# Kernel tuning notes

Measured on AMD Instinct MI355X. Metric: run time of the kernel, lower is better.

The kernel has to match this reference:

```python
import jax, jax.numpy as jnp
import numpy as np

B, S, D, FF, E = 4, 2048, 1024, 4096, 8


def setup_inputs() -> dict:
    key = jax.random.key(0)
    ks = jax.random.split(key, 6)
    scale_r = 1.0 / np.sqrt(D)
    return {
        "x": jax.random.normal(ks[0], (B, S, D), dtype=jnp.float32),
        "W_router": jax.random.normal(ks[1], (D, E), dtype=jnp.float32) * scale_r,
        "W1": jax.random.normal(ks[2], (E, D, FF), dtype=jnp.float32) * (1.0 / np.sqrt(D)),
        "b1": jnp.zeros((E, FF), dtype=jnp.float32),
        "W2": jax.random.normal(ks[3], (E, FF, D), dtype=jnp.float32) * (1.0 / np.sqrt(FF)),
        "b2": jnp.zeros((E, D), dtype=jnp.float32),
    }


def reference(x, W_router, W1, b1, W2, b2):
    # Router: softmax over experts, top-2, renormalize the 2 gates with softmax
    logits = jnp.einsum("bsd,de->bse", x, W_router)          # [B,S,E]
    probs = jax.nn.softmax(logits, axis=-1)
    top_vals, top_idx = jax.lax.top_k(probs, 2)               # [B,S,2]
    gates2 = jax.nn.softmax(top_vals, axis=-1)                # [B,S,2]

    num_experts = W1.shape[0]
    out = jnp.zeros_like(x)
    # Faithful masked-dense MoE: each expert runs over all tokens (input masked),
    # output scaled by its gate (0 for non-selected tokens).
    for i in range(num_experts):
        sel = (top_idx == i)                                  # [B,S,2] bool
        mask = jnp.any(sel, axis=-1, keepdims=True).astype(x.dtype)  # [B,S,1]
        xi = x * mask
        h = jax.nn.gelu(jnp.einsum("bsd,df->bsf", xi, W1[i]) + b1[i], approximate=False)
        yi = jnp.einsum("bsf,fd->bsd", h, W2[i]) + b2[i]
        g = jnp.sum(gates2 * sel.astype(x.dtype), axis=-1, keepdims=True)  # [B,S,1]
        out = out + yi * g
    return out
```

## Files before the change

kernel.cpp:

```cpp
#include <hip/hip_runtime.h>
#include <hip/hip_bf16.h>
#include <math.h>

#define NEXP 8
#define DDIM 1024
#define FFDIM 4096
#define NTOK 8192
#define NSLOT (NTOK * 2)
#define BM 128
#define BN 128
#define BK 64
#define MAXT ((NSLOT / BM) + NEXP)

typedef __attribute__((ext_vector_type(8))) __bf16 bf16x8;
typedef __attribute__((ext_vector_type(4))) float f32x4;

union BF8 { __bf16 b[8]; uint4 u; bf16x8 v; };

__device__ __forceinline__ float gelu_exact(float v) {
    return 0.5f * v * (1.0f + erff(v * 0.70710678118654752f));
}

__device__ __forceinline__ int swz(int row, int colb) {
    return row * 128 + (colb ^ ((row & 7) << 4));
}

__global__ __launch_bounds__(64)
void router_kernel(const float* __restrict__ x, const float* __restrict__ Wr,
                   int* __restrict__ idx2, float* __restrict__ gates2,
                   int* __restrict__ counts)
{
    int t = blockIdx.x;
    int lane = threadIdx.x;
    const float* xr = x + (size_t)t * DDIM;
    float acc[NEXP];
#pragma unroll
    for (int e = 0; e < NEXP; ++e) acc[e] = 0.f;
    for (int d = lane; d < DDIM; d += 64) {
        float xv = xr[d];
        const float* wrow = Wr + d * NEXP;
#pragma unroll
        for (int e = 0; e < NEXP; ++e) acc[e] += xv * wrow[e];
    }
#pragma unroll
    for (int e = 0; e < NEXP; ++e) {
        float v = acc[e];
        for (int off = 32; off > 0; off >>= 1) v += __shfl_xor(v, off, 64);
        acc[e] = v;
    }
    if (lane == 0) {
        float mx = acc[0];
#pragma unroll
        for (int e = 1; e < NEXP; ++e) mx = fmaxf(mx, acc[e]);
        float p[NEXP]; float s = 0.f;
#pragma unroll
        for (int e = 0; e < NEXP; ++e) { p[e] = expf(acc[e] - mx); s += p[e]; }
        float inv = 1.f / s;
#pragma unroll
        for (int e = 0; e < NEXP; ++e) p[e] *= inv;
        int i1 = 0; float p1 = p[0];
#pragma unroll
        for (int e = 1; e < NEXP; ++e) if (p[e] > p1) { p1 = p[e]; i1 = e; }
        int i2 = -1; float p2 = -1.f;
#pragma unroll
        for (int e = 0; e < NEXP; ++e) {
            if (e == i1) continue;
            if (p[e] > p2) { p2 = p[e]; i2 = e; }
        }
        float u = expf(p2 - p1);
        float den = 1.f + u;
        idx2[2 * t] = i1; idx2[2 * t + 1] = i2;
        gates2[2 * t] = 1.f / den; gates2[2 * t + 1] = u / den;
        atomicAdd(&counts[i1], 1);
        atomicAdd(&counts[i2], 1);
    }
}

__global__ void offsets_kernel(const int* __restrict__ counts, int* __restrict__ offsets,
                               int* __restrict__ cursors, int* __restrict__ tiletab)
{
    if (threadIdx.x != 0 || blockIdx.x != 0) return;
    int off = 0, idx = 0;
    for (int e = 0; e < NEXP; ++e) {
        offsets[e] = off;
        cursors[e] = 0;
        int nt = (counts[e] + BM - 1) / BM;
        for (int t = 0; t < nt; ++t) { tiletab[2 * idx] = e; tiletab[2 * idx + 1] = t; ++idx; }
        off += counts[e];
    }
    for (; idx < MAXT; ++idx) { tiletab[2 * idx] = -1; tiletab[2 * idx + 1] = 0; }
}

__global__ __launch_bounds__(256)
void fill_kernel(const int* __restrict__ idx2, const float* __restrict__ gates2,
                 const int* __restrict__ offsets, int* __restrict__ cursors,
                 int* __restrict__ perm, float* __restrict__ gate_slot)
{
    int t = blockIdx.x * 256 + threadIdx.x;
    if (t >= NTOK) return;
#pragma unroll
    for (int s = 0; s < 2; ++s) {
        int e = idx2[2 * t + s];
        int pos = atomicAdd(&cursors[e], 1);
        int slot = offsets[e] + pos;
        perm[slot] = t;
        gate_slot[slot] = gates2[2 * t + s];
    }
}

__global__ __launch_bounds__(256)
void convert_x_kernel(const float* __restrict__ x, __bf16* __restrict__ xb)
{
    size_t i = ((size_t)blockIdx.x * 256 + threadIdx.x) * 8;
    float4 a = *(const float4*)(x + i);
    float4 b = *(const float4*)(x + i + 4);
    BF8 pk;
    pk.b[0] = (__bf16)a.x; pk.b[1] = (__bf16)a.y; pk.b[2] = (__bf16)a.z; pk.b[3] = (__bf16)a.w;
    pk.b[4] = (__bf16)b.x; pk.b[5] = (__bf16)b.y; pk.b[6] = (__bf16)b.z; pk.b[7] = (__bf16)b.w;
    *(uint4*)(xb + i) = pk.u;
}

__global__ __launch_bounds__(256)
void convert_w_kernel(const float* __restrict__ W, __bf16* __restrict__ WT, int K, int N)
{
    int ktiles = K >> 6;
    int nt = blockIdx.x / ktiles;
    int kt = blockIdx.x % ktiles;
    int e = blockIdx.y;
    const float* We = W + (size_t)e * K * N;
    int t = threadIdx.x;
    int r = t & 127;
    int khalf = t >> 7;
    const float* src = We + (size_t)(kt * 64 + khalf * 32) * N + nt * 128 + r;
    char* dst = (char*)WT + ((((size_t)e * (N >> 7) + nt) * ktiles + kt) << 14);
    float f[32];
#pragma unroll
    for (int j = 0; j < 32; ++j) f[j] = src[(size_t)j * N];
#pragma unroll
    for (int i = 0; i < 4; ++i) {
        BF8 pk;
#pragma unroll
        for (int q = 0; q < 8; ++q) pk.b[q] = (__bf16)f[i * 8 + q];
        int gi = khalf * 4 + i;
        *(uint4*)(dst + r * 128 + ((gi * 16) ^ ((r & 7) << 4))) = pk.u;
    }
}

__device__ __forceinline__ bool tile_header(const int* counts, const int* offsets,
                                            const int* tiletab, int e_arg, int c_arg, int CH,
                                            int& e, int& start, int& cnt, int& hbase, int& row0,
                                            int& rows_here)
{
    int rowtile;
    if (e_arg >= 0) {
        e = e_arg;
        int cbase = c_arg * CH;
        cnt = counts[e] - cbase;
        if (cnt <= 0) return false;
        if (cnt > CH) cnt = CH;
        start = offsets[e] + cbase;
        rowtile = blockIdx.y;
        hbase = start;
    } else {
        e = tiletab[2 * blockIdx.y];
        if (e < 0) return false;
        rowtile = tiletab[2 * blockIdx.y + 1];
        start = offsets[e];
        cnt = counts[e];
        hbase = 0;
    }
    row0 = rowtile * BM;
    if (row0 >= cnt) return false;
    rows_here = cnt - row0;
    if (rows_here > BM) rows_here = BM;
    return true;
}

__global__ __launch_bounds__(256)
void gemm1_fast(const __bf16* __restrict__ xb, const __bf16* __restrict__ W1T,
                const float* __restrict__ b1,
                const int* __restrict__ perm, const int* __restrict__ counts,
                const int* __restrict__ offsets, const int* __restrict__ tiletab,
                __bf16* __restrict__ H, int e_arg, int c_arg, int CH)
{
    __shared__ __align__(16) char smem[(BM + BN) * 128];
    char* As = smem;
    char* Bs = smem + BM * 128;

    int e, start, cnt, hbase, row0, rows_here;
    if (!tile_header(counts, offsets, tiletab, e_arg, c_arg, CH, e, start, cnt, hbase, row0, rows_here))
        return;

    const float* b1e = b1 + (size_t)e * FFDIM;
    int nt = blockIdx.x;
    int n0 = nt * BN;
    const char* bsrc = (const char*)W1T + ((((size_t)e * (FFDIM >> 7) + nt) * (DDIM >> 6)) << 14);

    int tid = threadIdx.x;
    int lane = tid & 63;
    int wid = tid >> 6;
    int wm = wid >> 1, wn = wid & 1;
    int lr = lane & 15, lhi = lane >> 4;

    int ar = tid >> 1, ach = tid & 1;
    int token = -1;
    if (ar < rows_here) token = perm[start + row0 + ar];
    const __bf16* arow = xb + (size_t)(token < 0 ? 0 : token) * DDIM + ach * 32;

    int boff = wid * 4096 + lane * 16;

    f32x4 acc[4][4] = {};

    for (int kt = 0; kt < DDIM / BK; ++kt) {
        __syncthreads();
        {
            uint4 v[4];
            if (token >= 0) {
                const uint4* p = (const uint4*)(arow + kt * BK);
#pragma unroll
                for (int i = 0; i < 4; ++i) v[i] = p[i];
            } else {
#pragma unroll
                for (int i = 0; i < 4; ++i) v[i] = make_uint4(0u, 0u, 0u, 0u);
            }
#pragma unroll
            for (int i = 0; i < 4; ++i)
                *(uint4*)(As + swz(ar, ach * 64 + i * 16)) = v[i];
        }
        {
            const char* tsrc = bsrc + ((size_t)kt << 14);
#pragma unroll
            for (int j = 0; j < 4; ++j) {
                uint4 v = *(const uint4*)(tsrc + j * 1024 + boff);
                *(uint4*)(Bs + j * 1024 + boff) = v;
            }
        }
        __syncthreads();

#pragma unroll
        for (int kk = 0; kk < 2; ++kk) {
            bf16x8 af[4], bfr[4];
#pragma unroll
            for (int m = 0; m < 4; ++m)
                af[m] = *(const bf16x8*)(As + swz(wm * 64 + m * 16 + lr, kk * 64 + lhi * 16));
#pragma unroll
            for (int n = 0; n < 4; ++n)
                bfr[n] = *(const bf16x8*)(Bs + swz(wn * 64 + n * 16 + lr, kk * 64 + lhi * 16));
#pragma unroll
            for (int m = 0; m < 4; ++m)
#pragma unroll
                for (int n = 0; n < 4; ++n)
                    acc[m][n] = __builtin_amdgcn_mfma_f32_16x16x32_bf16(af[m], bfr[n], acc[m][n], 0, 0, 0);
        }
    }

    float bias[4];
#pragma unroll
    for (int n = 0; n < 4; ++n) bias[n] = b1e[n0 + wn * 64 + n * 16 + lr];

#pragma unroll
    for (int m = 0; m < 4; ++m) {
        int rbase = wm * 64 + m * 16 + lhi * 4;
#pragma unroll
        for (int j = 0; j < 4; ++j) {
            int rl = rbase + j;
            if (rl < rows_here) {
                __bf16* hr = H + (size_t)(start + row0 + rl - hbase) * FFDIM + n0 + wn * 64;
#pragma unroll
                for (int n = 0; n < 4; ++n) {
                    float v = acc[m][n][j] + bias[n];
                    hr[n * 16 + lr] = (__bf16)gelu_exact(v);
                }
            }
        }
    }
}

__global__ __launch_bounds__(256)
void gemm2_fast(const __bf16* __restrict__ H, const __bf16* __restrict__ W2T,
                const float* __restrict__ b2,
                const int* __restrict__ perm, const float* __restrict__ gate_slot,
                const int* __restrict__ counts, const int* __restrict__ offsets,
                const int* __restrict__ tiletab,
                float* __restrict__ out, int e_arg, int c_arg, int CH)
{
    __shared__ __align__(16) char smem[(BM + BN) * 128];
    char* As = smem;
    char* Bs = smem + BM * 128;

    int e, start, cnt, hbase, row0, rows_here;
    if (!tile_header(counts, offsets, tiletab, e_arg, c_arg, CH, e, start, cnt, hbase, row0, rows_here))
        return;

    const float* b2e = b2 + (size_t)e * DDIM;
    int nt = blockIdx.x;
    int n0 = nt * BN;
    const char* bsrc = (const char*)W2T + ((((size_t)e * (DDIM >> 7) + nt) * (FFDIM >> 6)) << 14);

    int tid = threadIdx.x;
    int lane = tid & 63;
    int wid = tid >> 6;
    int wm = wid >> 1, wn = wid & 1;
    int lr = lane & 15, lhi = lane >> 4;

    int ar = tid >> 1, ach = tid & 1;
    bool aval = (ar < rows_here);
    const __bf16* hrow = H + (size_t)(aval ? (start + row0 + ar - hbase) : 0) * FFDIM + ach * 32;

    int boff = wid * 4096 + lane * 16;

    f32x4 acc[4][4] = {};

    for (int kt = 0; kt < FFDIM / BK; ++kt) {
        __syncthreads();
        {
            uint4 v[4];
            if (aval) {
                const uint4* p = (const uint4*)(hrow + kt * BK);
#pragma unroll
                for (int i = 0; i < 4; ++i) v[i] = p[i];
            } else {
#pragma unroll
                for (int i = 0; i < 4; ++i) v[i] = make_uint4(0u, 0u, 0u, 0u);
            }
#pragma unroll
            for (int i = 0; i < 4; ++i)
                *(uint4*)(As + swz(ar, ach * 64 + i * 16)) = v[i];
        }
        {
            const char* tsrc = bsrc + ((size_t)kt << 14);
#pragma unroll
            for (int j = 0; j < 4; ++j) {
                uint4 v = *(const uint4*)(tsrc + j * 1024 + boff);
                *(uint4*)(Bs + j * 1024 + boff) = v;
            }
        }
        __syncthreads();

#pragma unroll
        for (int kk = 0; kk < 2; ++kk) {
            bf16x8 af[4], bfr[4];
#pragma unroll
            for (int m = 0; m < 4; ++m)
                af[m] = *(const bf16x8*)(As + swz(wm * 64 + m * 16 + lr, kk * 64 + lhi * 16));
#pragma unroll
            for (int n = 0; n < 4; ++n)
                bfr[n] = *(const bf16x8*)(Bs + swz(wn * 64 + n * 16 + lr, kk * 64 + lhi * 16));
#pragma unroll
            for (int m = 0; m < 4; ++m)
#pragma unroll
                for (int n = 0; n < 4; ++n)
                    acc[m][n] = __builtin_amdgcn_mfma_f32_16x16x32_bf16(af[m], bfr[n], acc[m][n], 0, 0, 0);
        }
    }

    float bias[4];
#pragma unroll
    for (int n = 0; n < 4; ++n) bias[n] = b2e[n0 + wn * 64 + n * 16 + lr];

#pragma unroll
    for (int m = 0; m < 4; ++m) {
        int rbase = wm * 64 + m * 16 + lhi * 4;
#pragma unroll
        for (int j = 0; j < 4; ++j) {
            int rl = rbase + j;
            if (rl < rows_here) {
                int slot = start + row0 + rl;
                int token = perm[slot];
                float g = gate_slot[slot];
                float* orow = out + (size_t)token * DDIM + n0 + wn * 64;
#pragma unroll
                for (int n = 0; n < 4; ++n) {
                    float v = (acc[m][n][j] + bias[n]) * g;
                    atomicAdd(orow + n * 16 + lr, v);
                }
            }
        }
    }
}

__global__ __launch_bounds__(256)
void gemm1_legacy(const float* __restrict__ x, const float* __restrict__ W1,
                  const float* __restrict__ b1,
                  const int* __restrict__ perm, const int* __restrict__ counts,
                  const int* __restrict__ offsets, const int* __restrict__ tiletab,
                  __bf16* __restrict__ H, int e_arg, int c_arg, int CH)
{
    __shared__ __align__(16) char smem[(BM + BN) * 128];
    char* As = smem;
    char* Bs = smem + BM * 128;

    int e, start, cnt, hbase, row0, rows_here;
    if (!tile_header(counts, offsets, tiletab, e_arg, c_arg, CH, e, start, cnt, hbase, row0, rows_here))
        return;

    const float* W1e = W1 + (size_t)e * DDIM * FFDIM;
    const float* b1e = b1 + (size_t)e * FFDIM;
    int n0 = blockIdx.x * BN;

    int tid = threadIdx.x;
    int lane = tid & 63;
    int wid = tid >> 6;
    int wm = wid >> 1, wn = wid & 1;
    int lr = lane & 15, lhi = lane >> 4;

    int ar = tid >> 1, ach = tid & 1;
    int token = -1;
    if (ar < rows_here) token = perm[start + row0 + ar];
    const float* arow = x + (size_t)(token < 0 ? 0 : token) * DDIM + ach * 32;

    int bn = tid & 127, bkh = tid >> 7;
    const float* bcol = W1e + (size_t)bkh * 32 * FFDIM + n0 + bn;

    f32x4 acc[4][4] = {};

    for (int k0 = 0; k0 < DDIM; k0 += BK) {
        __syncthreads();
        {
            BF8 pk[4];
            if (token >= 0) {
                const float4* p = (const float4*)(arow + k0);
#pragma unroll
                for (int i = 0; i < 4; ++i) {
                    float4 v0 = p[2 * i], v1 = p[2 * i + 1];
                    pk[i].b[0] = (__bf16)v0.x; pk[i].b[1] = (__bf16)v0.y;
                    pk[i].b[2] = (__bf16)v0.z; pk[i].b[3] = (__bf16)v0.w;
                    pk[i].b[4] = (__bf16)v1.x; pk[i].b[5] = (__bf16)v1.y;
                    pk[i].b[6] = (__bf16)v1.z; pk[i].b[7] = (__bf16)v1.w;
                }
            } else {
#pragma unroll
                for (int i = 0; i < 4; ++i) pk[i].u = make_uint4(0u, 0u, 0u, 0u);
            }
#pragma unroll
            for (int i = 0; i < 4; ++i)
                *(uint4*)(As + swz(ar, ach * 64 + i * 16)) = pk[i].u;
        }
        {
            float f[32];
            const float* p = bcol + (size_t)k0 * FFDIM;
#pragma unroll
            for (int j = 0; j < 32; ++j) f[j] = p[(size_t)j * FFDIM];
#pragma unroll
            for (int i = 0; i < 4; ++i) {
                BF8 pk;
#pragma unroll
                for (int q = 0; q < 8; ++q) pk.b[q] = (__bf16)f[i * 8 + q];
                *(uint4*)(Bs + swz(bn, bkh * 64 + i * 16)) = pk.u;
            }
        }
        __syncthreads();

#pragma unroll
        for (int kk = 0; kk < 2; ++kk) {
            bf16x8 af[4], bfr[4];
#pragma unroll
            for (int m = 0; m < 4; ++m)
                af[m] = *(const bf16x8*)(As + swz(wm * 64 + m * 16 + lr, kk * 64 + lhi * 16));
#pragma unroll
            for (int n = 0; n < 4; ++n)
                bfr[n] = *(const bf16x8*)(Bs + swz(wn * 64 + n * 16 + lr, kk * 64 + lhi * 16));
#pragma unroll
            for (int m = 0; m < 4; ++m)
#pragma unroll
                for (int n = 0; n < 4; ++n)
                    acc[m][n] = __builtin_amdgcn_mfma_f32_16x16x32_bf16(af[m], bfr[n], acc[m][n], 0, 0, 0);
        }
    }

    float bias[4];
#pragma unroll
    for (int n = 0; n < 4; ++n) bias[n] = b1e[n0 + wn * 64 + n * 16 + lr];

#pragma unroll
    for (int m = 0; m < 4; ++m) {
        int rbase = wm * 64 + m * 16 + lhi * 4;
#pragma unroll
        for (int j = 0; j < 4; ++j) {
            int rl = rbase + j;
            if (rl < rows_here) {
                __bf16* hr = H + (size_t)(start + row0 + rl - hbase) * FFDIM + n0 + wn * 64;
#pragma unroll
                for (int n = 0; n < 4; ++n) {
                    float v = acc[m][n][j] + bias[n];
                    hr[n * 16 + lr] = (__bf16)gelu_exact(v);
                }
            }
        }
    }
}

__global__ __launch_bounds__(256)
void gemm2_legacy(const __bf16* __restrict__ H, const float* __restrict__ W2,
                  const float* __restrict__ b2,
                  const int* __restrict__ perm, const float* __restrict__ gate_slot,
                  const int* __restrict__ counts, const int* __restrict__ offsets,
                  const int* __restrict__ tiletab,
                  float* __restrict__ out, int e_arg, int c_arg, int CH)
{
    __shared__ __align__(16) char smem[(BM + BN) * 128];
    char* As = smem;
    char* Bs = smem + BM * 128;

    int e, start, cnt, hbase, row0, rows_here;
    if (!tile_header(counts, offsets, tiletab, e_arg, c_arg, CH, e, start, cnt, hbase, row0, rows_here))
        return;

    const float* W2e = W2 + (size_t)e * FFDIM * DDIM;
    const float* b2e = b2 + (size_t)e * DDIM;
    int n0 = blockIdx.x * BN;

    int tid = threadIdx.x;
    int lane = tid & 63;
    int wid = tid >> 6;
    int wm = wid >> 1, wn = wid & 1;
    int lr = lane & 15, lhi = lane >> 4;

    int ar = tid >> 1, ach = tid & 1;
    bool aval = (ar < rows_here);
    const __bf16* hrow = H + (size_t)(aval ? (start + row0 + ar - hbase) : 0) * FFDIM + ach * 32;

    int bn = tid & 127, bkh = tid >> 7;
    const float* bcol = W2e + (size_t)bkh * 32 * DDIM + n0 + bn;

    f32x4 acc[4][4] = {};

    for (int k0 = 0; k0 < FFDIM; k0 += BK) {
        __syncthreads();
        {
            uint4 v[4];
            if (aval) {
                const uint4* p = (const uint4*)(hrow + k0);
#pragma unroll
                for (int i = 0; i < 4; ++i) v[i] = p[i];
            } else {
#pragma unroll
                for (int i = 0; i < 4; ++i) v[i] = make_uint4(0u, 0u, 0u, 0u);
            }
#pragma unroll
            for (int i = 0; i < 4; ++i)
                *(uint4*)(As + swz(ar, ach * 64 + i * 16)) = v[i];
        }
        {
            float f[32];
            const float* p = bcol + (size_t)k0 * DDIM;
#pragma unroll
            for (int j = 0; j < 32; ++j) f[j] = p[(size_t)j * DDIM];
#pragma unroll
            for (int i = 0; i < 4; ++i) {
                BF8 pk;
#pragma unroll
                for (int q = 0; q < 8; ++q) pk.b[q] = (__bf16)f[i * 8 + q];
                *(uint4*)(Bs + swz(bn, bkh * 64 + i * 16)) = pk.u;
            }
        }
        __syncthreads();

#pragma unroll
        for (int kk = 0; kk < 2; ++kk) {
            bf16x8 af[4], bfr[4];
#pragma unroll
            for (int m = 0; m < 4; ++m)
                af[m] = *(const bf16x8*)(As + swz(wm * 64 + m * 16 + lr, kk * 64 + lhi * 16));
#pragma unroll
            for (int n = 0; n < 4; ++n)
                bfr[n] = *(const bf16x8*)(Bs + swz(wn * 64 + n * 16 + lr, kk * 64 + lhi * 16));
#pragma unroll
            for (int m = 0; m < 4; ++m)
#pragma unroll
                for (int n = 0; n < 4; ++n)
                    acc[m][n] = __builtin_amdgcn_mfma_f32_16x16x32_bf16(af[m], bfr[n], acc[m][n], 0, 0, 0);
        }
    }

    float bias[4];
#pragma unroll
    for (int n = 0; n < 4; ++n) bias[n] = b2e[n0 + wn * 64 + n * 16 + lr];

#pragma unroll
    for (int m = 0; m < 4; ++m) {
        int rbase = wm * 64 + m * 16 + lhi * 4;
#pragma unroll
        for (int j = 0; j < 4; ++j) {
            int rl = rbase + j;
            if (rl < rows_here) {
                int slot = start + row0 + rl;
                int token = perm[slot];
                float g = gate_slot[slot];
                float* orow = out + (size_t)token * DDIM + n0 + wn * 64;
#pragma unroll
                for (int n = 0; n < 4; ++n) {
                    float v = (acc[m][n][j] + bias[n]) * g;
                    atomicAdd(orow + n * 16 + lr, v);
                }
            }
        }
    }
}

extern "C" void kernel_launch(void* const* d_in, const int* in_sizes, int n_in,
                              void* d_out, int out_size, void* d_ws, size_t ws_size,
                              hipStream_t stream)
{
    const float* x  = (const float*)d_in[0];
    const float* Wr = (const float*)d_in[1];
    const float* W1 = (const float*)d_in[2];
    const float* b1 = (const float*)d_in[3];
    const float* W2 = (const float*)d_in[4];
    const float* b2 = (const float*)d_in[5];
    float* out = (float*)d_out;

    char* ws = (char*)d_ws;
    int* counts   = (int*)ws;
    int* offsets  = counts + 8;
    int* cursors  = offsets + 8;
    int* tiletab  = cursors + 8;
    int* idx2     = tiletab + 2 * MAXT;
    float* gates2 = (float*)(idx2 + 2 * NTOK);
    int* perm     = (int*)(gates2 + 2 * NTOK);
    float* gate_slot = (float*)(perm + NSLOT);
    char* hraw = (char*)(gate_slot + NSLOT);
    size_t small_end = (((size_t)(hraw - ws)) + 255) & ~(size_t)255;

    __bf16* xb  = (__bf16*)(ws + small_end);
    __bf16* W1T = xb + (size_t)NTOK * DDIM;
    __bf16* W2T = W1T + (size_t)NEXP * DDIM * FFDIM;
    __bf16* Hf  = W2T + (size_t)NEXP * FFDIM * DDIM;
    size_t fast_off = small_end + ((size_t)NTOK * DDIM + 2 * (size_t)NEXP * DDIM * FFDIM) * 2;
    size_t availHf = ws_size > fast_off ? ws_size - fast_off : 0;
    size_t need_H = (size_t)NSLOT * FFDIM * 2;
    bool have_w = availHf >= (size_t)BM * FFDIM * 2 * 8;

    hipMemsetAsync(d_out, 0, (size_t)out_size * sizeof(float), stream);
    hipMemsetAsync(counts, 0, 8 * sizeof(int), stream);

    router_kernel<<<NTOK, 64, 0, stream>>>(x, Wr, idx2, gates2, counts);
    if (have_w) {
        convert_x_kernel<<<NTOK * DDIM / 2048, 256, 0, stream>>>(x, xb);
        convert_w_kernel<<<dim3((FFDIM / 128) * (DDIM / 64), NEXP), 256, 0, stream>>>(W1, W1T, DDIM, FFDIM);
        convert_w_kernel<<<dim3((DDIM / 128) * (FFDIM / 64), NEXP), 256, 0, stream>>>(W2, W2T, FFDIM, DDIM);
    }
    offsets_kernel<<<1, 1, 0, stream>>>(counts, offsets, cursors, tiletab);
    fill_kernel<<<NTOK / 256, 256, 0, stream>>>(idx2, gates2, offsets, cursors, perm, gate_slot);

    if (have_w && availHf >= need_H) {
        dim3 g1(FFDIM / BN, MAXT, 1);
        gemm1_fast<<<g1, 256, 0, stream>>>(xb, W1T, b1, perm, counts, offsets, tiletab, Hf, -1, 0, 0);
        dim3 g2(DDIM / BN, MAXT, 1);
        gemm2_fast<<<g2, 256, 0, stream>>>(Hf, W2T, b2, perm, gate_slot, counts, offsets, tiletab, out, -1, 0, 0);
    } else if (have_w) {
        long long chl = (long long)((availHf / ((size_t)FFDIM * 2)) / BM) * BM;
        int CH = (int)(chl > 4096 ? 4096 : chl);
        int nchunk = (NSLOT + CH - 1) / CH;
        for (int e = 0; e < NEXP; ++e) {
            for (int c = 0; c < nchunk; ++c) {
                dim3 g1(FFDIM / BN, CH / BM, 1);
                gemm1_fast<<<g1, 256, 0, stream>>>(xb, W1T, b1, perm, counts, offsets, tiletab, Hf, e, c, CH);
                dim3 g2(DDIM / BN, CH / BM, 1);
                gemm2_fast<<<g2, 256, 0, stream>>>(Hf, W2T, b2, perm, gate_slot, counts, offsets, tiletab, out, e, c, CH);
            }
        }
    } else {
        __bf16* H = (__bf16*)(ws + small_end);
        size_t avail = ws_size > small_end ? ws_size - small_end : 0;
        if (avail >= need_H) {
            dim3 g1(FFDIM / BN, MAXT, 1);
            gemm1_legacy<<<g1, 256, 0, stream>>>(x, W1, b1, perm, counts, offsets, tiletab, H, -1, 0, 0);
            dim3 g2(DDIM / BN, MAXT, 1);
            gemm2_legacy<<<g2, 256, 0, stream>>>(H, W2, b2, perm, gate_slot, counts, offsets, tiletab, out, -1, 0, 0);
        } else {
            long long chl = (long long)((avail / ((size_t)FFDIM * 2)) / BM) * BM;
            int CH = (int)(chl > 2048 ? 2048 : chl);
            if (CH >= BM) {
                int nchunk = (NSLOT + CH - 1) / CH;
                for (int e = 0; e < NEXP; ++e) {
                    for (int c = 0; c < nchunk; ++c) {
                        dim3 g1(FFDIM / BN, CH / BM, 1);
                        gemm1_legacy<<<g1, 256, 0, stream>>>(x, W1, b1, perm, counts, offsets, tiletab, H, e, c, CH);
                        dim3 g2(DDIM / BN, CH / BM, 1);
                        gemm2_legacy<<<g2, 256, 0, stream>>>(H, W2, b2, perm, gate_slot, counts, offsets, tiletab, out, e, c, CH);
                    }
                }
            }
        }
    }
}
```

Measured before the change: 856.2 us.

## Use direct global-to-LDS loads in expert GEMMs and replace atomics with combine pass

GEMM tile loads now use global_load_lds so data goes straight from global memory into shared memory without staging in registers. The second GEMM writes gated per-slot outputs into a scratch buffer, reusing the no-longer-needed W1T space, and a new combine kernel sums the two slots per token. This removes the float atomics and the output memset. The offsets kernel is parallelised and the weight conversion kernel is restructured to use 128 threads with 64 rows each. The combine pass adds an extra read of the per-slot output and write of the final output.

```diff
diff --git a/kernel.cpp b/kernel.cpp
--- a/kernel.cpp
+++ b/kernel.cpp
@@ -25,6 +25,12 @@
     return row * 128 + (colb ^ ((row & 7) << 4));
 }
 
+typedef const __attribute__((address_space(1))) void* gptr1_t;
+typedef __attribute__((address_space(3))) void* lptr3_t;
+__device__ __forceinline__ void gll16(const void* g, void* l) {
+    __builtin_amdgcn_global_load_lds((gptr1_t)g, (lptr3_t)l, 16, 0, 0);
+}
+
 __global__ __launch_bounds__(64)
 void router_kernel(const float* __restrict__ x, const float* __restrict__ Wr,
                    int* __restrict__ idx2, float* __restrict__ gates2,
@@ -76,25 +82,40 @@
     }
 }
 
-__global__ void offsets_kernel(const int* __restrict__ counts, int* __restrict__ offsets,
-                               int* __restrict__ cursors, int* __restrict__ tiletab)
-{
-    if (threadIdx.x != 0 || blockIdx.x != 0) return;
-    int off = 0, idx = 0;
-    for (int e = 0; e < NEXP; ++e) {
-        offsets[e] = off;
-        cursors[e] = 0;
-        int nt = (counts[e] + BM - 1) / BM;
-        for (int t = 0; t < nt; ++t) { tiletab[2 * idx] = e; tiletab[2 * idx + 1] = t; ++idx; }
-        off += counts[e];
-    }
-    for (; idx < MAXT; ++idx) { tiletab[2 * idx] = -1; tiletab[2 * idx + 1] = 0; }
+__global__ __launch_bounds__(256)
+void offsets_kernel(const int* __restrict__ counts, int* __restrict__ offsets,
+                    int* __restrict__ cursors, int* __restrict__ tiletab)
+{
+    __shared__ int soff[NEXP], stile[NEXP + 1];
+    int tid = threadIdx.x;
+    if (tid == 0) {
+        int off = 0, tt = 0;
+        for (int e = 0; e < NEXP; ++e) {
+            soff[e] = off; stile[e] = tt;
+            int c = counts[e];
+            off += c; tt += (c + BM - 1) / BM;
+        }
+        stile[NEXP] = tt;
+    }
+    __syncthreads();
+    if (tid < NEXP) { offsets[tid] = soff[tid]; cursors[tid] = 0; }
+    int total = stile[NEXP];
+    for (int i = tid; i < MAXT; i += 256) {
+        if (i < total) {
+            int e = 0;
+            while (stile[e + 1] <= i) ++e;
+            tiletab[2 * i] = e; tiletab[2 * i + 1] = i - stile[e];
+        } else {
+            tiletab[2 * i] = -1; tiletab[2 * i + 1] = 0;
+        }
+    }
 }
 
 __global__ __launch_bounds__(256)
 void fill_kernel(const int* __restrict__ idx2, const float* __restrict__ gates2,
                  const int* __restrict__ offsets, int* __restrict__ cursors,
-                 int* __restrict__ perm, float* __restrict__ gate_slot)
+                 int* __restrict__ perm, float* __restrict__ gate_slot,
+                 int* __restrict__ tslot)
 {
     int t = blockIdx.x * 256 + threadIdx.x;
     if (t >= NTOK) return;
@@ -105,6 +126,7 @@
         int slot = offsets[e] + pos;
         perm[slot] = t;
         gate_slot[slot] = gates2[2 * t + s];
+        tslot[2 * t + s] = slot;
     }
 }
 
@@ -120,7 +142,7 @@
     *(uint4*)(xb + i) = pk.u;
 }
 
-__global__ __launch_bounds__(256)
+__global__ __launch_bounds__(128)
 void convert_w_kernel(const float* __restrict__ W, __bf16* __restrict__ WT, int K, int N)
 {
     int ktiles = K >> 6;
@@ -128,21 +150,18 @@
     int kt = blockIdx.x % ktiles;
     int e = blockIdx.y;
     const float* We = W + (size_t)e * K * N;
-    int t = threadIdx.x;
-    int r = t & 127;
-    int khalf = t >> 7;
-    const float* src = We + (size_t)(kt * 64 + khalf * 32) * N + nt * 128 + r;
-    char* dst = (char*)WT + ((((size_t)e * (N >> 7) + nt) * ktiles + kt) << 14);
-    float f[32];
-#pragma unroll
-    for (int j = 0; j < 32; ++j) f[j] = src[(size_t)j * N];
-#pragma unroll
-    for (int i = 0; i < 4; ++i) {
+    int r = threadIdx.x;
+    const float* src = We + (size_t)(kt * 64) * N + nt * 128 + r;
+    char* dst = (char*)WT + ((((size_t)e * (N >> 7) + nt) * ktiles + kt) << 14) + r * 128;
+    float f[64];
+#pragma unroll
+    for (int j = 0; j < 64; ++j) f[j] = src[(size_t)j * N];
+#pragma unroll
+    for (int gi = 0; gi < 8; ++gi) {
         BF8 pk;
 #pragma unroll
-        for (int q = 0; q < 8; ++q) pk.b[q] = (__bf16)f[i * 8 + q];
-        int gi = khalf * 4 + i;
-        *(uint4*)(dst + r * 128 + ((gi * 16) ^ ((r & 7) << 4))) = pk.u;
+        for (int q = 0; q < 8; ++q) pk.b[q] = (__bf16)f[gi * 8 + q];
+        *(uint4*)(dst + ((gi * 16) ^ ((r & 7) << 4))) = pk.u;
     }
 }
 
@@ -202,39 +221,29 @@
     int wm = wid >> 1, wn = wid & 1;
     int lr = lane & 15, lhi = lane >> 4;
 
-    int ar = tid >> 1, ach = tid & 1;
-    int token = -1;
-    if (ar < rows_here) token = perm[start + row0 + ar];
-    const __bf16* arow = xb + (size_t)(token < 0 ? 0 : token) * DDIM + ach * 32;
-
-    int boff = wid * 4096 + lane * 16;
+    int laneswz = (((lane & 7) ^ (lane >> 3)) << 4);
+    const char* xrowp[4];
+#pragma unroll
+    for (int j = 0; j < 4; ++j) {
+        int rr = wid * 32 + j * 8 + (lane >> 3);
+        int re = rr < rows_here ? rr : 0;
+        int tok = perm[start + row0 + re];
+        xrowp[j] = (const char*)(xb + (size_t)tok * DDIM);
+    }
+    char* aldsb = As + wid * 4096;
+    char* bldsb = Bs + wid * 4096;
+    const char* bwave = bsrc + wid * 4096 + lane * 16;
 
     f32x4 acc[4][4] = {};
 
     for (int kt = 0; kt < DDIM / BK; ++kt) {
         __syncthreads();
-        {
-            uint4 v[4];
-            if (token >= 0) {
-                const uint4* p = (const uint4*)(arow + kt * BK);
-#pragma unroll
-                for (int i = 0; i < 4; ++i) v[i] = p[i];
-            } else {
-#pragma unroll
-                for (int i = 0; i < 4; ++i) v[i] = make_uint4(0u, 0u, 0u, 0u);
-            }
-#pragma unroll
-            for (int i = 0; i < 4; ++i)
-                *(uint4*)(As + swz(ar, ach * 64 + i * 16)) = v[i];
-        }
-        {
-            const char* tsrc = bsrc + ((size_t)kt << 14);
-#pragma unroll
-            for (int j = 0; j < 4; ++j) {
-                uint4 v = *(const uint4*)(tsrc + j * 1024 + boff);
-                *(uint4*)(Bs + j * 1024 + boff) = v;
-            }
-        }
+#pragma unroll
+        for (int j = 0; j < 4; ++j)
+            gll16(xrowp[j] + kt * 128 + laneswz, aldsb + j * 1024);
+#pragma unroll
+        for (int j = 0; j < 4; ++j)
+            gll16(bwave + ((size_t)kt << 14) + j * 1024, bldsb + j * 1024);
         __syncthreads();
 
 #pragma unroll
@@ -282,7 +291,8 @@
                 const int* __restrict__ perm, const float* __restrict__ gate_slot,
                 const int* __restrict__ counts, const int* __restrict__ offsets,
                 const int* __restrict__ tiletab,
-                float* __restrict__ out, int e_arg, int c_arg, int CH)
+                float* __restrict__ out, float* __restrict__ Y, int use_y,
+                int e_arg, int c_arg, int CH)
 {
     __shared__ __align__(16) char smem[(BM + BN) * 128];
     char* As = smem;
@@ -303,38 +313,28 @@
     int wm = wid >> 1, wn = wid & 1;
     int lr = lane & 15, lhi = lane >> 4;
 
-    int ar = tid >> 1, ach = tid & 1;
-    bool aval = (ar < rows_here);
-    const __bf16* hrow = H + (size_t)(aval ? (start + row0 + ar - hbase) : 0) * FFDIM + ach * 32;
-
-    int boff = wid * 4096 + lane * 16;
+    int laneswz = (((lane & 7) ^ (lane >> 3)) << 4);
+    const char* hrowp[4];
+#pragma unroll
+    for (int j = 0; j < 4; ++j) {
+        int rr = wid * 32 + j * 8 + (lane >> 3);
+        int re = rr < rows_here ? rr : 0;
+        hrowp[j] = (const char*)(H + (size_t)(start + row0 + re - hbase) * FFDIM);
+    }
+    char* aldsb = As + wid * 4096;
+    char* bldsb = Bs + wid * 4096;
+    const char* bwave = bsrc + wid * 4096 + lane * 16;
 
     f32x4 acc[4][4] = {};
 
     for (int kt = 0; kt < FFDIM / BK; ++kt) {
         __syncthreads();
-        {
-            uint4 v[4];
-            if (aval) {
-                const uint4* p = (const uint4*)(hrow + kt * BK);
-#pragma unroll
-                for (int i = 0; i < 4; ++i) v[i] = p[i];
-            } else {
-#pragma unroll
-                for (int i = 0; i < 4; ++i) v[i] = make_uint4(0u, 0u, 0u, 0u);
-            }
-#pragma unroll
-            for (int i = 0; i < 4; ++i)
-                *(uint4*)(As + swz(ar, ach * 64 + i * 16)) = v[i];
-        }
-        {
-            const char* tsrc = bsrc + ((size_t)kt << 14);
-#pragma unroll
-            for (int j = 0; j < 4; ++j) {
-                uint4 v = *(const uint4*)(tsrc + j * 1024 + boff);
-                *(uint4*)(Bs + j * 1024 + boff) = v;
-            }
-        }
+#pragma unroll
+        for (int j = 0; j < 4; ++j)
+            gll16(hrowp[j] + kt * 128 + laneswz, aldsb + j * 1024);
+#pragma unroll
+        for (int j = 0; j < 4; ++j)
+            gll16(bwave + ((size_t)kt << 14) + j * 1024, bldsb + j * 1024);
         __syncthreads();
 
 #pragma unroll
@@ -366,17 +366,36 @@
             int rl = rbase + j;
             if (rl < rows_here) {
                 int slot = start + row0 + rl;
-                int token = perm[slot];
                 float g = gate_slot[slot];
-                float* orow = out + (size_t)token * DDIM + n0 + wn * 64;
-#pragma unroll
-                for (int n = 0; n < 4; ++n) {
-                    float v = (acc[m][n][j] + bias[n]) * g;
-                    atomicAdd(orow + n * 16 + lr, v);
+                if (use_y) {
+                    float* yrow = Y + (size_t)slot * DDIM + n0 + wn * 64;
+#pragma unroll
+                    for (int n = 0; n < 4; ++n)
+                        yrow[n * 16 + lr] = (acc[m][n][j] + bias[n]) * g;
+                } else {
+                    int token = perm[slot];
+                    float* orow = out + (size_t)token * DDIM + n0 + wn * 64;
+#pragma unroll
+                    for (int n = 0; n < 4; ++n)
+                        atomicAdd(orow + n * 16 + lr, (acc[m][n][j] + bias[n]) * g);
                 }
             }
         }
     }
+}
+
+__global__ __launch_bounds__(256)
+void combine_kernel(const float* __restrict__ Y, const int* __restrict__ tslot,
+                    float* __restrict__ out)
+{
+    int t = blockIdx.x;
+    int c = threadIdx.x * 4;
+    int sa = tslot[2 * t], sb = tslot[2 * t + 1];
+    float4 a = *(const float4*)(Y + (size_t)sa * DDIM + c);
+    float4 b = *(const float4*)(Y + (size_t)sb * DDIM + c);
+    float4 r;
+    r.x = a.x + b.x; r.y = a.y + b.y; r.z = a.z + b.z; r.w = a.w + b.w;
+    *(float4*)(out + (size_t)t * DDIM + c) = r;
 }
 
 __global__ __launch_bounds__(256)
@@ -619,36 +638,40 @@
     float* gates2 = (float*)(idx2 + 2 * NTOK);
     int* perm     = (int*)(gates2 + 2 * NTOK);
     float* gate_slot = (float*)(perm + NSLOT);
-    char* hraw = (char*)(gate_slot + NSLOT);
+    int* tslot    = (int*)(gate_slot + NSLOT);
+    char* hraw = (char*)(tslot + 2 * NTOK);
     size_t small_end = (((size_t)(hraw - ws)) + 255) & ~(size_t)255;
 
     __bf16* xb  = (__bf16*)(ws + small_end);
     __bf16* W1T = xb + (size_t)NTOK * DDIM;
     __bf16* W2T = W1T + (size_t)NEXP * DDIM * FFDIM;
     __bf16* Hf  = W2T + (size_t)NEXP * FFDIM * DDIM;
+    float*  Y   = (float*)W1T;
     size_t fast_off = small_end + ((size_t)NTOK * DDIM + 2 * (size_t)NEXP * DDIM * FFDIM) * 2;
     size_t availHf = ws_size > fast_off ? ws_size - fast_off : 0;
     size_t need_H = (size_t)NSLOT * FFDIM * 2;
     bool have_w = availHf >= (size_t)BM * FFDIM * 2 * 8;
 
-    hipMemsetAsync(d_out, 0, (size_t)out_size * sizeof(float), stream);
     hipMemsetAsync(counts, 0, 8 * sizeof(int), stream);
 
     router_kernel<<<NTOK, 64, 0, stream>>>(x, Wr, idx2, gates2, counts);
     if (have_w) {
         convert_x_kernel<<<NTOK * DDIM / 2048, 256, 0, stream>>>(x, xb);
-        convert_w_kernel<<<dim3((FFDIM / 128) * (DDIM / 64), NEXP), 256, 0, stream>>>(W1, W1T, DDIM, FFDIM);
-        convert_w_kernel<<<dim3((DDIM / 128) * (FFDIM / 64), NEXP), 256, 0, stream>>>(W2, W2T, FFDIM, DDIM);
-    }
-    offsets_kernel<<<1, 1, 0, stream>>>(counts, offsets, cursors, tiletab);
-    fill_kernel<<<NTOK / 256, 256, 0, stream>>>(idx2, gates2, offsets, cursors, perm, gate_slot);
+        convert_w_kernel<<<dim3((FFDIM / 128) * (DDIM / 64), NEXP), 128, 0, stream>>>(W1, W1T, DDIM, FFDIM);
+        convert_w_kernel<<<dim3((DDIM / 128) * (FFDIM / 64), NEXP), 128, 0, stream>>>(W2, W2T, FFDIM, DDIM);
+    }
+    offsets_kernel<<<1, 256, 0, stream>>>(counts, offsets, cursors, tiletab);
+    fill_kernel<<<NTOK / 256, 256, 0, stream>>>(idx2, gates2, offsets, cursors, perm, gate_slot, tslot);
 
     if (have_w && availHf >= need_H) {
         dim3 g1(FFDIM / BN, MAXT, 1);
         gemm1_fast<<<g1, 256, 0, stream>>>(xb, W1T, b1, perm, counts, offsets, tiletab, Hf, -1, 0, 0);
         dim3 g2(DDIM / BN, MAXT, 1);
-        gemm2_fast<<<g2, 256, 0, stream>>>(Hf, W2T, b2, perm, gate_slot, counts, offsets, tiletab, out, -1, 0, 0);
+        gemm2_fast<<<g2, 256, 0, stream>>>(Hf, W2T, b2, perm, gate_slot, counts, offsets, tiletab,
+                                           out, Y, 1, -1, 0, 0);
+        combine_kernel<<<NTOK, 256, 0, stream>>>(Y, tslot, out);
     } else if (have_w) {
+        hipMemsetAsync(d_out, 0, (size_t)out_size * sizeof(float), stream);
         long long chl = (long long)((availHf / ((size_t)FFDIM * 2)) / BM) * BM;
         int CH = (int)(chl > 4096 ? 4096 : chl);
         int nchunk = (NSLOT + CH - 1) / CH;
@@ -657,10 +680,12 @@
                 dim3 g1(FFDIM / BN, CH / BM, 1);
                 gemm1_fast<<<g1, 256, 0, stream>>>(xb, W1T, b1, perm, counts, offsets, tiletab, Hf, e, c, CH);
                 dim3 g2(DDIM / BN, CH / BM, 1);
-                gemm2_fast<<<g2, 256, 0, stream>>>(Hf, W2T, b2, perm, gate_slot, counts, offsets, tiletab, out, e, c, CH);
+                gemm2_fast<<<g2, 256, 0, stream>>>(Hf, W2T, b2, perm, gate_slot, counts, offsets, tiletab,
+                                                   out, (float*)nullptr, 0, e, c, CH);
             }
         }
     } else {
+        hipMemsetAsync(d_out, 0, (size_t)out_size * sizeof(float), stream);
         __bf16* H = (__bf16*)(ws + small_end);
         size_t avail = ws_size > small_end ? ws_size - small_end : 0;
         if (avail >= need_H) {
```

New measurement: 956.4 us. 1.12x slower.
